# Kernel optimization log

Hardware: AMD Instinct MI355X
Metric: run time of the kernel (lower is better)

## Reference

```python
import jax, jax.numpy as jnp
import numpy as np


def setup_inputs() -> dict:
    key = jax.random.key(0)
    ks = jax.random.split(key, 8)
    B, S, K, D = 2, 64, 64, 256
    C = D // 8
    return {
        "x": jax.random.normal(ks[0], (B, S, K, D), dtype=jnp.float32),
        "Wq": jax.random.normal(ks[1], (C, D), dtype=jnp.float32) * (1.0 / np.sqrt(D)),
        "bq": jax.random.normal(ks[2], (C,), dtype=jnp.float32) * 0.01,
        "Wk": jax.random.normal(ks[3], (C, D), dtype=jnp.float32) * (1.0 / np.sqrt(D)),
        "bk": jax.random.normal(ks[4], (C,), dtype=jnp.float32) * 0.01,
        "Wv": jax.random.normal(ks[5], (D, D), dtype=jnp.float32) * (1.0 / np.sqrt(D)),
        "bv": jax.random.normal(ks[6], (D,), dtype=jnp.float32) * 0.01,
        "gamma": jax.random.uniform(ks[7], (1,), dtype=jnp.float32),
    }


def reference(x, Wq, bq, Wk, bk, Wv, bv, gamma):
    # x: [B, S, K, D]
    B, S, K, D = x.shape
    N = K * S
    # torch: x.permute(0,3,2,1) -> [B, D, K, S]; flatten (K,S) -> N (n = k*S + s)
    xp = jnp.transpose(x, (0, 3, 2, 1)).reshape(B, D, N)  # [B, D, N]
    # 1x1 convs == per-token linear maps over the channel dim
    q = jnp.einsum('cd,bdn->bnc', Wq, xp) + bq            # [B, N, C]
    k = jnp.einsum('cd,bdn->bcn', Wk, xp) + bk[:, None]   # [B, C, N]
    energy = jnp.einsum('bnc,bcm->bnm', q, k)             # [B, N, N]
    attention = jax.nn.softmax(energy, axis=-1)           # rows sum to 1
    v = jnp.einsum('ed,bdn->ben', Wv, xp) + bv[:, None]   # [B, D, N]
    # out[b,d,i] = sum_j V[b,d,j] * A[b,i,j]
    out = jnp.einsum('bdj,bij->bdi', v, attention)        # [B, D, N]
    out = gamma * out + xp                                # residual with learned scale
    out = out.reshape(B, D, K, S)
    return jnp.transpose(out, (0, 3, 2, 1))               # [B, S, K, D]
```

## Files before the change

kernel.cpp:

```cpp
#include <hip/hip_runtime.h>
#include <stdint.h>
#include <math.h>

using short8   = __attribute__((ext_vector_type(8))) short;
using ushort4v = __attribute__((ext_vector_type(4))) unsigned short;
using f32x4    = __attribute__((ext_vector_type(4))) float;
using uint4v   = __attribute__((ext_vector_type(4))) unsigned int;

#define B_ 2
#define S_ 64
#define K_ 64
#define D_ 256
#define C_ 32
#define N_ 4096
#define LOG2E 1.4426950408889634f

__device__ __forceinline__ float b2f(unsigned short u) {
    unsigned int v = ((unsigned int)u) << 16;
    return __builtin_bit_cast(float, v);
}
__device__ __forceinline__ unsigned short f2b(float f) {
    unsigned int x = __builtin_bit_cast(unsigned int, f);
    x += 0x7fffu + ((x >> 16) & 1u);
    return (unsigned short)(x >> 16);
}
__device__ __forceinline__ unsigned int pk2(float a, float b) {
    unsigned int xa = __builtin_bit_cast(unsigned int, a);
    unsigned int xb = __builtin_bit_cast(unsigned int, b);
    xa += 0x7fffu + ((xa >> 16) & 1u);
    xb += 0x7fffu + ((xb >> 16) & 1u);
    return (xa >> 16) | (xb & 0xffff0000u);
}

__global__ __launch_bounds__(256) void wcvt_kernel(
    const float* __restrict__ Wq, const float* __restrict__ bq,
    const float* __restrict__ Wk, const float* __restrict__ bk,
    const float* __restrict__ Wv, const float* __restrict__ bv,
    unsigned short* __restrict__ Wh, unsigned short* __restrict__ Wl,
    float* __restrict__ bcat)
{
    int oc = blockIdx.x;
    int d  = threadIdx.x;
    float w;
    if (oc < 32)       w = Wq[oc * 256 + d] * LOG2E;
    else if (oc < 64)  w = Wk[(oc - 32) * 256 + d];
    else               w = Wv[(oc - 64) * 256 + d];
    unsigned short h = f2b(w);
    Wh[oc * 256 + d] = h;
    Wl[oc * 256 + d] = f2b(w - b2f(h));
    if (d == 0) {
        float bb;
        if (oc < 32)      bb = bq[oc] * LOG2E;
        else if (oc < 64) bb = bk[oc - 32];
        else              bb = bv[oc - 64];
        bcat[oc] = bb;
    }
}

__global__ __launch_bounds__(256) void qkv_kernel(
    const float* __restrict__ x,
    const unsigned short* __restrict__ Wh, const unsigned short* __restrict__ Wl,
    const float* __restrict__ bcat,
    unsigned short* __restrict__ Qh, unsigned short* __restrict__ Ql,
    unsigned short* __restrict__ Kh, unsigned short* __restrict__ Kl,
    unsigned short* __restrict__ Vm)
{
    __shared__ unsigned short lxh[16 * 256];
    __shared__ unsigned short lxl[16 * 256];

    int tid = threadIdx.x;
    int bid = blockIdx.x;
    int b  = bid >> 8;
    int n0 = (bid & 255) << 4;

    {
        int tt = tid >> 4, dg0 = (tid & 15) * 16;
        int n = n0 + tt;
        int s = n & 63, kk = n >> 6;
        const float* xr = x + (((size_t)(b * S_ + s)) * K_ + kk) * D_ + dg0;
        short8 h0, l0, h1, l1;
#pragma unroll
        for (int e = 0; e < 8; ++e) {
            float v = xr[e];
            unsigned short hh = f2b(v);
            h0[e] = (short)hh; l0[e] = (short)f2b(v - b2f(hh));
        }
#pragma unroll
        for (int e = 0; e < 8; ++e) {
            float v = xr[8 + e];
            unsigned short hh = f2b(v);
            h1[e] = (short)hh; l1[e] = (short)f2b(v - b2f(hh));
        }
        int m0 = dg0 >> 3;
        int sw0 = ((m0 ^ (tt & 7)) << 3);
        int sw1 = (((m0 + 1) ^ (tt & 7)) << 3);
        *(short8*)(lxh + tt * 256 + sw0) = h0;
        *(short8*)(lxh + tt * 256 + sw1) = h1;
        *(short8*)(lxl + tt * 256 + sw0) = l0;
        *(short8*)(lxl + tt * 256 + sw1) = l1;
    }
    __syncthreads();

    int wave = tid >> 6, lane = tid & 63;
    int col = lane & 15, g = lane >> 4;

#pragma unroll
    for (int i = 0; i < 5; ++i) {
        int ct = wave + i * 4;
        int oc0 = ct * 16;
        const unsigned short* whr = Wh + (size_t)(oc0 + col) * 256;
        const unsigned short* wlr = Wl + (size_t)(oc0 + col) * 256;
        f32x4 acc = {0.f, 0.f, 0.f, 0.f};

        if (ct < 4) {
#pragma unroll
            for (int dc = 0; dc < 8; ++dc) {
                int sw = (((dc * 4 + g) ^ (col & 7)) << 3);
                short8 xh8 = *(const short8*)(lxh + col * 256 + sw);
                short8 xl8 = *(const short8*)(lxl + col * 256 + sw);
                short8 wh8 = *(const short8*)(whr + dc * 32 + g * 8);
                short8 wl8 = *(const short8*)(wlr + dc * 32 + g * 8);
                acc = __builtin_amdgcn_mfma_f32_16x16x32_bf16(xl8, wh8, acc, 0, 0, 0);
                acc = __builtin_amdgcn_mfma_f32_16x16x32_bf16(xh8, wl8, acc, 0, 0, 0);
                acc = __builtin_amdgcn_mfma_f32_16x16x32_bf16(xh8, wh8, acc, 0, 0, 0);
            }
            float bb = bcat[oc0 + col];
            unsigned short* Th = (ct < 2) ? Qh : Kh;
            unsigned short* Tl = (ct < 2) ? Ql : Kl;
            int c0 = (ct & 1) * 16;
#pragma unroll
            for (int r = 0; r < 4; ++r) {
                int tok = n0 + g * 4 + r;
                float v = acc[r] + bb;
                unsigned short hh = f2b(v);
                size_t idx = ((size_t)b * N_ + tok) * C_ + c0 + col;
                Th[idx] = hh;
                Tl[idx] = f2b(v - b2f(hh));
            }
        } else {
#pragma unroll
            for (int dc = 0; dc < 8; ++dc) {
                int sw = (((dc * 4 + g) ^ (col & 7)) << 3);
                short8 xh8 = *(const short8*)(lxh + col * 256 + sw);
                short8 wh8 = *(const short8*)(whr + dc * 32 + g * 8);
                acc = __builtin_amdgcn_mfma_f32_16x16x32_bf16(xh8, wh8, acc, 0, 0, 0);
            }
            float bb = bcat[oc0 + col];
            int c0 = oc0 - 64;
            ushort4v st;
#pragma unroll
            for (int r = 0; r < 4; ++r) st[r] = f2b(acc[r] + bb);
            int tok0 = n0 + g * 4;
            int s0 = 8 * g + ((n0 & 16) >> 2);
            int d_ch = c0 + col;
            int o = d_ch * 64 + s0 * 2;
            o ^= (d_ch & 7) << 4;
            size_t vbyteoff = ((size_t)b * (N_ / 32) + (tok0 >> 5)) * (D_ * 32 * 2)
                            + (size_t)o;
            *(ushort4v*)((char*)Vm + vbyteoff) = st;
        }
    }
}

__global__ __launch_bounds__(512, 2) void attn_kernel(
    const unsigned short* __restrict__ Qh, const unsigned short* __restrict__ Ql,
    const unsigned short* __restrict__ Kh, const unsigned short* __restrict__ Kl,
    const unsigned short* __restrict__ Vm,
    float* __restrict__ O_part, float* __restrict__ lsum_part)
{
    __shared__ __align__(16) char vlds[2][16384];

    int tid  = threadIdx.x;
    int wave = tid >> 6;
    int lane = tid & 63;
    int col = lane & 15, g = lane >> 4;
    int qq = wave >> 1;
    int dh = wave & 1;
    int dbase = dh * 128;

    int bid = blockIdx.x;
    int x7 = bid & 7;
    int b  = x7 >> 2;
    int ks = x7 & 3;
    int qt = bid >> 3;
    int q0 = qt * 128 + qq * 32;
    int jbase = ks * (N_ / 4);

    size_t qoff0 = ((size_t)b * N_ + q0 + col) * C_ + g * 8;
    size_t qoff1 = ((size_t)b * N_ + q0 + 16 + col) * C_ + g * 8;
    short8 qfh0 = *(const short8*)(Qh + qoff0);
    short8 qfl0 = *(const short8*)(Ql + qoff0);
    short8 qfh1 = *(const short8*)(Qh + qoff1);
    short8 qfl1 = *(const short8*)(Ql + qoff1);

    f32x4 acc[2][8];
#pragma unroll
    for (int qs = 0; qs < 2; ++qs)
#pragma unroll
        for (int dt = 0; dt < 8; ++dt) acc[qs][dt] = (f32x4){0.f, 0.f, 0.f, 0.f};
    float l_run0 = 0.f, l_run1 = 0.f;

    const unsigned short* kbh = Kh + (size_t)b * N_ * C_;
    const unsigned short* kbl = Kl + (size_t)b * N_ * C_;
    const char* vbyte = (const char*)Vm + (size_t)b * ((size_t)N_ * D_ * 2);

    auto kaddr0 = [&](int it) { return (size_t)(jbase + it * 32 + col) * C_ + g * 8; };
    auto kaddr1 = [&](int it) { return (size_t)(jbase + it * 32 + 16 + col) * C_ + g * 8; };

    unsigned vro = (unsigned)(((dbase + col) * 64 + g * 16) ^ ((col & 7) << 4));

    {
        const char* vsrc = vbyte + (size_t)(ks * 32) * 16384 + tid * 16;
        f32x4 s0 = *(const f32x4*)(vsrc);
        f32x4 s1 = *(const f32x4*)(vsrc + 8192);
        *(f32x4*)(vlds[0] + tid * 16)        = s0;
        *(f32x4*)(vlds[0] + tid * 16 + 8192) = s1;
    }
    short8 kh0A = *(const short8*)(kbh + kaddr0(0));
    short8 kl0A = *(const short8*)(kbl + kaddr0(0));
    short8 kh1A = *(const short8*)(kbh + kaddr1(0));
    short8 kl1A = *(const short8*)(kbl + kaddr1(0));
    short8 kh0B, kl0B, kh1B, kl1B;
    __syncthreads();

#define ATTN_PHASE(IT, RB, WB, CKH0, CKL0, CKH1, CKL1, NKH0, NKL0, NKH1, NKL1)   \
    {                                                                            \
        int itn_ = (IT) + 1;                                                     \
        const char* vsrc_ = vbyte + (size_t)(ks * 32 + itn_) * 16384 + tid * 16; \
        f32x4 stg0_ = *(const f32x4*)(vsrc_);                                    \
        f32x4 stg1_ = *(const f32x4*)(vsrc_ + 8192);                             \
        NKH0 = *(const short8*)(kbh + kaddr0(itn_));                             \
        NKL0 = *(const short8*)(kbl + kaddr0(itn_));                             \
        NKH1 = *(const short8*)(kbh + kaddr1(itn_));                             \
        NKL1 = *(const short8*)(kbl + kaddr1(itn_));                             \
        __builtin_amdgcn_sched_barrier(0);        \
        f32x4 z_ = {0.f, 0.f, 0.f, 0.f};                                         \
        f32x4 s00 = __builtin_amdgcn_mfma_f32_16x16x32_bf16(CKL0, qfh0, z_, 0, 0, 0); \
        s00 = __builtin_amdgcn_mfma_f32_16x16x32_bf16(CKH0, qfl0, s00, 0, 0, 0); \
        s00 = __builtin_amdgcn_mfma_f32_16x16x32_bf16(CKH0, qfh0, s00, 0, 0, 0); \
        f32x4 s01 = __builtin_amdgcn_mfma_f32_16x16x32_bf16(CKL1, qfh0, z_, 0, 0, 0); \
        s01 = __builtin_amdgcn_mfma_f32_16x16x32_bf16(CKH1, qfl0, s01, 0, 0, 0); \
        s01 = __builtin_amdgcn_mfma_f32_16x16x32_bf16(CKH1, qfh0, s01, 0, 0, 0); \
        f32x4 s10 = __builtin_amdgcn_mfma_f32_16x16x32_bf16(CKL0, qfh1, z_, 0, 0, 0); \
        s10 = __builtin_amdgcn_mfma_f32_16x16x32_bf16(CKH0, qfl1, s10, 0, 0, 0); \
        s10 = __builtin_amdgcn_mfma_f32_16x16x32_bf16(CKH0, qfh1, s10, 0, 0, 0); \
        f32x4 s11 = __builtin_amdgcn_mfma_f32_16x16x32_bf16(CKL1, qfh1, z_, 0, 0, 0); \
        s11 = __builtin_amdgcn_mfma_f32_16x16x32_bf16(CKH1, qfl1, s11, 0, 0, 0); \
        s11 = __builtin_amdgcn_mfma_f32_16x16x32_bf16(CKH1, qfh1, s11, 0, 0, 0); \
        float pa[4], pc[4], pe[4], pg[4];                                        \
        _Pragma("unroll")                                                        \
        for (int r = 0; r < 4; ++r) {                                            \
            pa[r] = exp2f(s00[r]);                                               \
            pc[r] = exp2f(s01[r]);                                               \
            pe[r] = exp2f(s10[r]);                                               \
            pg[r] = exp2f(s11[r]);                                               \
        }                                                                        \
        l_run0 += (pa[0] + pa[1]) + (pa[2] + pa[3])                              \
                + (pc[0] + pc[1]) + (pc[2] + pc[3]);                             \
        l_run1 += (pe[0] + pe[1]) + (pe[2] + pe[3])                              \
                + (pg[0] + pg[1]) + (pg[2] + pg[3]);                             \
        uint4v u0, u1;                                                           \
        u0[0] = pk2(pa[0], pa[1]); u0[1] = pk2(pa[2], pa[3]);                    \
        u0[2] = pk2(pc[0], pc[1]); u0[3] = pk2(pc[2], pc[3]);                    \
        u1[0] = pk2(pe[0], pe[1]); u1[1] = pk2(pe[2], pe[3]);                    \
        u1[2] = pk2(pg[0], pg[1]); u1[3] = pk2(pg[2], pg[3]);                    \
        short8 pf0 = __builtin_bit_cast(short8, u0);                             \
        short8 pf1 = __builtin_bit_cast(short8, u1);                             \
        short8 vf_[8];                                                           \
        _Pragma("unroll")                                                        \
        for (int dt = 0; dt < 8; ++dt)                                           \
            vf_[dt] = *(const short8*)(vlds[RB] + vro + dt * 1024);              \
        _Pragma("unroll")                                                        \
        for (int dt = 0; dt < 8; ++dt) {                                         \
            acc[0][dt] = __builtin_amdgcn_mfma_f32_16x16x32_bf16(vf_[dt], pf0, acc[0][dt], 0, 0, 0); \
            acc[1][dt] = __builtin_amdgcn_mfma_f32_16x16x32_bf16(vf_[dt], pf1, acc[1][dt], 0, 0, 0); \
        }                                                                        \
        *(f32x4*)(vlds[WB] + tid * 16)        = stg0_;                           \
        *(f32x4*)(vlds[WB] + tid * 16 + 8192) = stg1_;                           \
        __syncthreads();                                                         \
    }

    for (int it2 = 0; it2 < 16; ++it2) {
        int itA = it2 * 2, itB = itA + 1;
        ATTN_PHASE(itA, 0, 1, kh0A, kl0A, kh1A, kl1A, kh0B, kl0B, kh1B, kl1B);
        ATTN_PHASE(itB, 1, 0, kh0B, kl0B, kh1B, kl1B, kh0A, kl0A, kh1A, kl1A);
    }
#undef ATTN_PHASE

    l_run0 += __shfl_xor(l_run0, 16); l_run0 += __shfl_xor(l_run0, 32);
    l_run1 += __shfl_xor(l_run1, 16); l_run1 += __shfl_xor(l_run1, 32);

    float* op = O_part + (size_t)bid * 32768 + wave * 4096;
#pragma unroll
    for (int qs = 0; qs < 2; ++qs)
#pragma unroll
        for (int dt = 0; dt < 8; ++dt) {
            int j = qs * 8 + dt;
            *(f32x4*)(op + j * 256 + col * 16 + g * 4) = acc[qs][dt];
        }
    if (dh == 0 && g == 0) {
        lsum_part[bid * 128 + qq * 32 + col]      = l_run0;
        lsum_part[bid * 128 + qq * 32 + 16 + col] = l_run1;
    }
}

__global__ __launch_bounds__(256) void epi_kernel(
    const float* __restrict__ O_part, const float* __restrict__ lsum_part,
    const float* __restrict__ x, const float* __restrict__ gamma_p,
    float* __restrict__ out)
{
    int gid = blockIdx.x * 256 + threadIdx.x;
    int d  = (gid & 63) * 4;
    int nl = gid >> 6;
    int b  = nl >> 12;
    int n  = nl & (N_ - 1);

    int qt = n >> 7, qq = (n >> 5) & 3, qs = (n >> 4) & 1, col = n & 15;
    int dh = d >> 7, dt = (d >> 4) & 7;
    int w = qq * 2 + dh, j = qs * 8 + dt;
    int boff = w * 4096 + j * 256 + col * 16 + (d & 15);
    int loff = qq * 32 + qs * 16 + col;

    f32x4 acc = {0.f, 0.f, 0.f, 0.f};
    float l = 0.f;
#pragma unroll
    for (int ks = 0; ks < 4; ++ks) {
        int bid = qt * 8 + b * 4 + ks;
        f32x4 p = *(const f32x4*)(O_part + (size_t)bid * 32768 + boff);
        acc[0] += p[0]; acc[1] += p[1]; acc[2] += p[2]; acc[3] += p[3];
        l += lsum_part[bid * 128 + loff];
    }
    float scale = gamma_p[0] / l;
    int s = n & 63, kk = n >> 6;
    size_t o = (((size_t)(b * S_ + s)) * K_ + kk) * D_ + d;
    f32x4 xv = *(const f32x4*)(x + o);
    f32x4 ov;
#pragma unroll
    for (int e = 0; e < 4; ++e) ov[e] = acc[e] * scale + xv[e];
    *(f32x4*)(out + o) = ov;
}

extern "C" void kernel_launch(void* const* d_in, const int* in_sizes, int n_in,
                              void* d_out, int out_size, void* d_ws, size_t ws_size,
                              hipStream_t stream) {
    const float* x  = (const float*)d_in[0];
    const float* Wq = (const float*)d_in[1];
    const float* bq = (const float*)d_in[2];
    const float* Wk = (const float*)d_in[3];
    const float* bk = (const float*)d_in[4];
    const float* Wv = (const float*)d_in[5];
    const float* bv = (const float*)d_in[6];
    const float* gm = (const float*)d_in[7];

    char* ws = (char*)d_ws;
    unsigned short* Wh   = (unsigned short*)(ws);
    unsigned short* Wl   = (unsigned short*)(ws + 0x40000);
    float*          bcat = (float*)         (ws + 0x80000);
    unsigned short* Qh   = (unsigned short*)(ws + 0x100000);
    unsigned short* Ql   = (unsigned short*)(ws + 0x180000);
    unsigned short* Kh   = (unsigned short*)(ws + 0x200000);
    unsigned short* Kl   = (unsigned short*)(ws + 0x280000);
    unsigned short* Vm   = (unsigned short*)(ws + 0x300000);
    float*          Op   = (float*)         (ws + 0x700000);
    float*          lp   = (float*)         (ws + 0x2700000);
    float* o = (float*)d_out;

    wcvt_kernel<<<320, 256, 0, stream>>>(Wq, bq, Wk, bk, Wv, bv, Wh, Wl, bcat);
    qkv_kernel<<<512, 256, 0, stream>>>(x, Wh, Wl, bcat, Qh, Ql, Kh, Kl, Vm);
    attn_kernel<<<256, 512, 0, stream>>>(Qh, Ql, Kh, Kl, Vm, Op, lp);
    epi_kernel<<<2048, 256, 0, stream>>>(Op, lp, x, gm, o);
}
```

Measured before the change: 77.01 us.

## Split QK^T score computation across wave pair and share P via LDS

```diff
diff --git a/kernel.cpp b/kernel.cpp
--- a/kernel.cpp
+++ b/kernel.cpp
@@ -169,6 +169,7 @@
     float* __restrict__ O_part, float* __restrict__ lsum_part)
 {
     __shared__ __align__(16) char vlds[2][16384];
+    __shared__ __align__(16) char plds[2 * 8192];
 
     int tid  = threadIdx.x;
     int wave = tid >> 6;
@@ -177,6 +178,8 @@
     int qq = wave >> 1;
     int dh = wave & 1;
     int dbase = dh * 128;
+    int tid16 = tid * 16;
+    int lane16 = lane * 16;
 
     int bid = blockIdx.x;
     int x7 = bid & 7;
@@ -186,19 +189,16 @@
     int q0 = qt * 128 + qq * 32;
     int jbase = ks * (N_ / 4);
 
-    size_t qoff0 = ((size_t)b * N_ + q0 + col) * C_ + g * 8;
-    size_t qoff1 = ((size_t)b * N_ + q0 + 16 + col) * C_ + g * 8;
-    short8 qfh0 = *(const short8*)(Qh + qoff0);
-    short8 qfl0 = *(const short8*)(Ql + qoff0);
-    short8 qfh1 = *(const short8*)(Qh + qoff1);
-    short8 qfl1 = *(const short8*)(Ql + qoff1);
+    size_t qoff = ((size_t)b * N_ + q0 + dh * 16 + col) * C_ + g * 8;
+    short8 qfh = *(const short8*)(Qh + qoff);
+    short8 qfl = *(const short8*)(Ql + qoff);
 
     f32x4 acc[2][8];
 #pragma unroll
     for (int qs = 0; qs < 2; ++qs)
 #pragma unroll
         for (int dt = 0; dt < 8; ++dt) acc[qs][dt] = (f32x4){0.f, 0.f, 0.f, 0.f};
-    float l_run0 = 0.f, l_run1 = 0.f;
+    float l_run = 0.f;
 
     const unsigned short* kbh = Kh + (size_t)b * N_ * C_;
     const unsigned short* kbl = Kl + (size_t)b * N_ * C_;
@@ -208,87 +208,112 @@
     auto kaddr1 = [&](int it) { return (size_t)(jbase + it * 32 + 16 + col) * C_ + g * 8; };
 
     unsigned vro = (unsigned)(((dbase + col) * 64 + g * 16) ^ ((col & 7) << 4));
+    char* pmy = plds + qq * 2048 + dh * 1024 + lane16;
+    const char* pr0 = plds + qq * 2048 + lane16;
+    const char* pr1 = plds + qq * 2048 + 1024 + lane16;
 
     {
-        const char* vsrc = vbyte + (size_t)(ks * 32) * 16384 + tid * 16;
+        const char* vsrc = vbyte + (size_t)(ks * 32) * 16384 + tid16;
         f32x4 s0 = *(const f32x4*)(vsrc);
         f32x4 s1 = *(const f32x4*)(vsrc + 8192);
-        *(f32x4*)(vlds[0] + tid * 16)        = s0;
-        *(f32x4*)(vlds[0] + tid * 16 + 8192) = s1;
+        *(f32x4*)(vlds[0] + tid16)        = s0;
+        *(f32x4*)(vlds[0] + tid16 + 8192) = s1;
     }
     short8 kh0A = *(const short8*)(kbh + kaddr0(0));
     short8 kl0A = *(const short8*)(kbl + kaddr0(0));
     short8 kh1A = *(const short8*)(kbh + kaddr1(0));
     short8 kl1A = *(const short8*)(kbl + kaddr1(0));
-    short8 kh0B, kl0B, kh1B, kl1B;
+    short8 kh0B = *(const short8*)(kbh + kaddr0(1));
+    short8 kl0B = *(const short8*)(kbl + kaddr0(1));
+    short8 kh1B = *(const short8*)(kbh + kaddr1(1));
+    short8 kl1B = *(const short8*)(kbl + kaddr1(1));
+    {
+        f32x4 z = {0.f, 0.f, 0.f, 0.f};
+        f32x4 sa = __builtin_amdgcn_mfma_f32_16x16x32_bf16(kl0A, qfh, z, 0, 0, 0);
+        sa = __builtin_amdgcn_mfma_f32_16x16x32_bf16(kh0A, qfl, sa, 0, 0, 0);
+        sa = __builtin_amdgcn_mfma_f32_16x16x32_bf16(kh0A, qfh, sa, 0, 0, 0);
+        f32x4 sb = __builtin_amdgcn_mfma_f32_16x16x32_bf16(kl1A, qfh, z, 0, 0, 0);
+        sb = __builtin_amdgcn_mfma_f32_16x16x32_bf16(kh1A, qfl, sb, 0, 0, 0);
+        sb = __builtin_amdgcn_mfma_f32_16x16x32_bf16(kh1A, qfh, sb, 0, 0, 0);
+        float pa[4], pb[4];
+#pragma unroll
+        for (int r = 0; r < 4; ++r) { pa[r] = exp2f(sa[r]); pb[r] = exp2f(sb[r]); }
+        l_run += (pa[0] + pa[1]) + (pa[2] + pa[3]) + (pb[0] + pb[1]) + (pb[2] + pb[3]);
+        uint4v uo;
+        uo[0] = pk2(pa[0], pa[1]); uo[1] = pk2(pa[2], pa[3]);
+        uo[2] = pk2(pb[0], pb[1]); uo[3] = pk2(pb[2], pb[3]);
+        *(uint4v*)(pmy) = uo;
+    }
     __syncthreads();
 
-#define ATTN_PHASE(IT, RB, WB, CKH0, CKL0, CKH1, CKL1, NKH0, NKL0, NKH1, NKL1)   \
+#define ATTN_PHASE(IT, CKH0, CKL0, CKH1, CKL1, NKH0, NKL0, NKH1, NKL1)           \
     {                                                                            \
         int itn_ = (IT) + 1;                                                     \
-        const char* vsrc_ = vbyte + (size_t)(ks * 32 + itn_) * 16384 + tid * 16; \
+        int itk_ = (IT) + 2;         \
+        const char* vsrc_ = vbyte + (size_t)(ks * 32 + itn_) * 16384 + tid16;    \
         f32x4 stg0_ = *(const f32x4*)(vsrc_);                                    \
         f32x4 stg1_ = *(const f32x4*)(vsrc_ + 8192);                             \
-        NKH0 = *(const short8*)(kbh + kaddr0(itn_));                             \
-        NKL0 = *(const short8*)(kbl + kaddr0(itn_));                             \
-        NKH1 = *(const short8*)(kbh + kaddr1(itn_));                             \
-        NKL1 = *(const short8*)(kbl + kaddr1(itn_));                             \
+        NKH0 = *(const short8*)(kbh + kaddr0(itk_));                             \
+        NKL0 = *(const short8*)(kbl + kaddr0(itk_));                             \
+        NKH1 = *(const short8*)(kbh + kaddr1(itk_));                             \
+        NKL1 = *(const short8*)(kbl + kaddr1(itk_));                             \
         __builtin_amdgcn_sched_barrier(0);        \
         f32x4 z_ = {0.f, 0.f, 0.f, 0.f};                                         \
-        f32x4 s00 = __builtin_amdgcn_mfma_f32_16x16x32_bf16(CKL0, qfh0, z_, 0, 0, 0); \
-        s00 = __builtin_amdgcn_mfma_f32_16x16x32_bf16(CKH0, qfl0, s00, 0, 0, 0); \
-        s00 = __builtin_amdgcn_mfma_f32_16x16x32_bf16(CKH0, qfh0, s00, 0, 0, 0); \
-        f32x4 s01 = __builtin_amdgcn_mfma_f32_16x16x32_bf16(CKL1, qfh0, z_, 0, 0, 0); \
-        s01 = __builtin_amdgcn_mfma_f32_16x16x32_bf16(CKH1, qfl0, s01, 0, 0, 0); \
-        s01 = __builtin_amdgcn_mfma_f32_16x16x32_bf16(CKH1, qfh0, s01, 0, 0, 0); \
-        f32x4 s10 = __builtin_amdgcn_mfma_f32_16x16x32_bf16(CKL0, qfh1, z_, 0, 0, 0); \
-        s10 = __builtin_amdgcn_mfma_f32_16x16x32_bf16(CKH0, qfl1, s10, 0, 0, 0); \
-        s10 = __builtin_amdgcn_mfma_f32_16x16x32_bf16(CKH0, qfh1, s10, 0, 0, 0); \
-        f32x4 s11 = __builtin_amdgcn_mfma_f32_16x16x32_bf16(CKL1, qfh1, z_, 0, 0, 0); \
-        s11 = __builtin_amdgcn_mfma_f32_16x16x32_bf16(CKH1, qfl1, s11, 0, 0, 0); \
-        s11 = __builtin_amdgcn_mfma_f32_16x16x32_bf16(CKH1, qfh1, s11, 0, 0, 0); \
-        float pa[4], pc[4], pe[4], pg[4];                                        \
+        f32x4 sa_ = __builtin_amdgcn_mfma_f32_16x16x32_bf16(CKL0, qfh, z_, 0, 0, 0); \
+        sa_ = __builtin_amdgcn_mfma_f32_16x16x32_bf16(CKH0, qfl, sa_, 0, 0, 0);  \
+        sa_ = __builtin_amdgcn_mfma_f32_16x16x32_bf16(CKH0, qfh, sa_, 0, 0, 0);  \
+        f32x4 sb_ = __builtin_amdgcn_mfma_f32_16x16x32_bf16(CKL1, qfh, z_, 0, 0, 0); \
+        sb_ = __builtin_amdgcn_mfma_f32_16x16x32_bf16(CKH1, qfl, sb_, 0, 0, 0);  \
+        sb_ = __builtin_amdgcn_mfma_f32_16x16x32_bf16(CKH1, qfh, sb_, 0, 0, 0);  \
+        float pa_[4], pb_[4];                                                    \
         _Pragma("unroll")                                                        \
-        for (int r = 0; r < 4; ++r) {                                            \
-            pa[r] = exp2f(s00[r]);                                               \
-            pc[r] = exp2f(s01[r]);                                               \
-            pe[r] = exp2f(s10[r]);                                               \
-            pg[r] = exp2f(s11[r]);                                               \
-        }                                                                        \
-        l_run0 += (pa[0] + pa[1]) + (pa[2] + pa[3])                              \
-                + (pc[0] + pc[1]) + (pc[2] + pc[3]);                             \
-        l_run1 += (pe[0] + pe[1]) + (pe[2] + pe[3])                              \
-                + (pg[0] + pg[1]) + (pg[2] + pg[3]);                             \
-        uint4v u0, u1;                                                           \
-        u0[0] = pk2(pa[0], pa[1]); u0[1] = pk2(pa[2], pa[3]);                    \
-        u0[2] = pk2(pc[0], pc[1]); u0[3] = pk2(pc[2], pc[3]);                    \
-        u1[0] = pk2(pe[0], pe[1]); u1[1] = pk2(pe[2], pe[3]);                    \
-        u1[2] = pk2(pg[0], pg[1]); u1[3] = pk2(pg[2], pg[3]);                    \
-        short8 pf0 = __builtin_bit_cast(short8, u0);                             \
-        short8 pf1 = __builtin_bit_cast(short8, u1);                             \
+        for (int r = 0; r < 4; ++r) { pa_[r] = exp2f(sa_[r]); pb_[r] = exp2f(sb_[r]); } \
+        l_run += (pa_[0] + pa_[1]) + (pa_[2] + pa_[3])                           \
+               + (pb_[0] + pb_[1]) + (pb_[2] + pb_[3]);                          \
+        uint4v uo_;                                                              \
+        uo_[0] = pk2(pa_[0], pa_[1]); uo_[1] = pk2(pa_[2], pa_[3]);              \
+        uo_[2] = pk2(pb_[0], pb_[1]); uo_[3] = pk2(pb_[2], pb_[3]);              \
+        int rb_ = (IT) & 1, wb_ = (itn_) & 1;                                    \
+        short8 pf0_ = *(const short8*)(pr0 + rb_ * 8192);                        \
+        short8 pf1_ = *(const short8*)(pr1 + rb_ * 8192);                        \
         short8 vf_[8];                                                           \
         _Pragma("unroll")                                                        \
         for (int dt = 0; dt < 8; ++dt)                                           \
-            vf_[dt] = *(const short8*)(vlds[RB] + vro + dt * 1024);              \
+            vf_[dt] = *(const short8*)(vlds[rb_] + vro + dt * 1024);             \
         _Pragma("unroll")                                                        \
         for (int dt = 0; dt < 8; ++dt) {                                         \
-            acc[0][dt] = __builtin_amdgcn_mfma_f32_16x16x32_bf16(vf_[dt], pf0, acc[0][dt], 0, 0, 0); \
-            acc[1][dt] = __builtin_amdgcn_mfma_f32_16x16x32_bf16(vf_[dt], pf1, acc[1][dt], 0, 0, 0); \
+            acc[0][dt] = __builtin_amdgcn_mfma_f32_16x16x32_bf16(vf_[dt], pf0_, acc[0][dt], 0, 0, 0); \
+            acc[1][dt] = __builtin_amdgcn_mfma_f32_16x16x32_bf16(vf_[dt], pf1_, acc[1][dt], 0, 0, 0); \
         }                                                                        \
-        *(f32x4*)(vlds[WB] + tid * 16)        = stg0_;                           \
-        *(f32x4*)(vlds[WB] + tid * 16 + 8192) = stg1_;                           \
+        *(uint4v*)(pmy + wb_ * 8192) = uo_;                                      \
+        *(f32x4*)(vlds[wb_] + tid16)        = stg0_;                             \
+        *(f32x4*)(vlds[wb_] + tid16 + 8192) = stg1_;                             \
         __syncthreads();                                                         \
     }
 
-    for (int it2 = 0; it2 < 16; ++it2) {
+    for (int it2 = 0; it2 < 15; ++it2) {
         int itA = it2 * 2, itB = itA + 1;
-        ATTN_PHASE(itA, 0, 1, kh0A, kl0A, kh1A, kl1A, kh0B, kl0B, kh1B, kl1B);
-        ATTN_PHASE(itB, 1, 0, kh0B, kl0B, kh1B, kl1B, kh0A, kl0A, kh1A, kl1A);
-    }
+        ATTN_PHASE(itA, kh0B, kl0B, kh1B, kl1B, kh0A, kl0A, kh1A, kl1A);
+        ATTN_PHASE(itB, kh0A, kl0A, kh1A, kl1A, kh0B, kl0B, kh1B, kl1B);
+    }
+    ATTN_PHASE(30, kh0B, kl0B, kh1B, kl1B, kh0A, kl0A, kh1A, kl1A);
 #undef ATTN_PHASE
 
-    l_run0 += __shfl_xor(l_run0, 16); l_run0 += __shfl_xor(l_run0, 32);
-    l_run1 += __shfl_xor(l_run1, 16); l_run1 += __shfl_xor(l_run1, 32);
+    {
+        short8 pf0 = *(const short8*)(pr0 + 8192);
+        short8 pf1 = *(const short8*)(pr1 + 8192);
+        short8 vf[8];
+#pragma unroll
+        for (int dt = 0; dt < 8; ++dt)
+            vf[dt] = *(const short8*)(vlds[1] + vro + dt * 1024);
+#pragma unroll
+        for (int dt = 0; dt < 8; ++dt) {
+            acc[0][dt] = __builtin_amdgcn_mfma_f32_16x16x32_bf16(vf[dt], pf0, acc[0][dt], 0, 0, 0);
+            acc[1][dt] = __builtin_amdgcn_mfma_f32_16x16x32_bf16(vf[dt], pf1, acc[1][dt], 0, 0, 0);
+        }
+    }
+
+    l_run += __shfl_xor(l_run, 16); l_run += __shfl_xor(l_run, 32);
 
     float* op = O_part + (size_t)bid * 32768 + wave * 4096;
 #pragma unroll
@@ -298,10 +323,8 @@
             int j = qs * 8 + dt;
             *(f32x4*)(op + j * 256 + col * 16 + g * 4) = acc[qs][dt];
         }
-    if (dh == 0 && g == 0) {
-        lsum_part[bid * 128 + qq * 32 + col]      = l_run0;
-        lsum_part[bid * 128 + qq * 32 + 16 + col] = l_run1;
-    }
+    if (g == 0)
+        lsum_part[bid * 128 + qq * 32 + dh * 16 + col] = l_run;
 }
 
 __global__ __launch_bounds__(256) void epi_kernel(
```

After: 69.44 us. 9.8% less time.
